# Kernel tuning notes

Measured on AMD Instinct MI355X. Metric: run time of the kernel, lower is better.

## Reference

```python
import jax, jax.numpy as jnp
import numpy as np
import math

B, P, N = 4, 8, 512
D_MODEL, H, D_K = 128, 4, 32
T_ALL = 4
WHICH_IDX = np.array([0, 1, 3])  # which_transition_matrices = [T,T,F,T]
T = 3
EPS = 1e-5


def setup_inputs() -> dict:
    key = jax.random.key(0)
    ks = jax.random.split(key, 12)
    inputs = jax.random.normal(ks[0], (B, P, N, D_MODEL), jnp.float32)
    c_inputs = jax.random.normal(ks[1], (B, P, N, D_MODEL), jnp.float32)
    vals = jax.random.uniform(ks[2], (T_ALL, N, N), jnp.float32)
    keep = (jax.random.uniform(ks[3], (T_ALL, N, N)) < 0.05).astype(jnp.float32)
    eye = jnp.eye(N, dtype=jnp.float32)
    transition_matrices = vals * keep * (1.0 - eye) + eye
    s = 1.0 / math.sqrt(D_MODEL)
    Wq = jax.random.normal(ks[4], (T, D_MODEL, D_MODEL), jnp.float32) * s
    Wk = jax.random.normal(ks[5], (T, D_MODEL, D_MODEL), jnp.float32) * s
    Wv = jax.random.normal(ks[6], (T, D_MODEL, D_MODEL), jnp.float32) * s
    Wo = jax.random.normal(ks[7], (D_MODEL, T * D_MODEL), jnp.float32) * (1.0 / math.sqrt(T * D_MODEL))
    ln_gamma = jnp.ones((D_MODEL,), jnp.float32)
    ln_beta = jnp.zeros((D_MODEL,), jnp.float32)
    return dict(inputs=inputs, c_inputs=c_inputs, transition_matrices=transition_matrices,
                Wq=Wq, Wk=Wk, Wv=Wv, Wo=Wo, ln_gamma=ln_gamma, ln_beta=ln_beta)


def reference(inputs, c_inputs, transition_matrices, Wq, Wk, Wv, Wo, ln_gamma, ln_beta):
    tm = transition_matrices[jnp.asarray(WHICH_IDX)]  # [T, N, N]
    # per-transition-matrix projections (torch Linear: x @ W.T), then split heads
    def proj(W):
        y = jnp.einsum('bpnd,tod->tbpno', inputs, W)
        return y.reshape(T, B, P, N, H, D_K)
    Q, K, V = proj(Wq), proj(Wk), proj(Wv)
    scores = jnp.einsum('tbpnhk,tbpmhk->tbphnm', Q, K) / math.sqrt(D_K)
    mask = jnp.where(tm != 0, 0.0, -jnp.inf)[:, None, None, None]  # [T,1,1,1,N,N]
    alpha = jax.nn.softmax(scores + mask, axis=-1)
    # post-softmax reweighting by transition matrix, then V matmul
    out = jnp.einsum('tbphnm,tbpmhk->tbpnhk', alpha * tm[:, None, None, None], V)
    out = out.reshape(T, B, P, N, D_MODEL)
    out = jnp.moveaxis(out, 0, -2).reshape(B, P, N, T * D_MODEL)  # concat over matrices
    out = jnp.einsum('bpnf,df->bpnd', out, Wo)  # final Linear (bias=False); dropout p=0
    res = out + inputs
    mu = res.mean(-1, keepdims=True)
    var = ((res - mu) ** 2).mean(-1, keepdims=True)
    return (res - mu) / jnp.sqrt(var + EPS) * ln_gamma + ln_beta
```

## Files before the change

kernel.cpp:

```cpp
#include <hip/hip_runtime.h>


typedef __attribute__((ext_vector_type(8))) short  short8;
typedef __attribute__((ext_vector_type(4))) float  floatx4;

#define WS_BIG   50331648ull
#define WS_XL    54919168ull
#define QSCALE   0.25503486f

__device__ __forceinline__ float b2f(unsigned short u) {
    union { unsigned int i; float f; } v; v.i = ((unsigned int)u) << 16; return v.f;
}
__device__ __forceinline__ unsigned short f2b(float f) {
    union { float f; unsigned int i; } v; v.f = f;
    unsigned int x = v.i;
    return (unsigned short)((x + 0x7fffu + ((x >> 16) & 1u)) >> 16);
}
__device__ __forceinline__ unsigned int fbits(float f) {
    union { float f; unsigned int i; } v; v.f = f; return v.i;
}
__device__ __forceinline__ short8 cvt8(const float* p) {
    floatx4 a = *(const floatx4*)p;
    floatx4 b = *(const floatx4*)(p + 4);
    short8 r;
    r[0] = (short)f2b(a[0]); r[1] = (short)f2b(a[1]);
    r[2] = (short)f2b(a[2]); r[3] = (short)f2b(a[3]);
    r[4] = (short)f2b(b[0]); r[5] = (short)f2b(b[1]);
    r[6] = (short)f2b(b[2]); r[7] = (short)f2b(b[3]);
    return r;
}

__global__ __launch_bounds__(256) void k_prep_w(
    const float* __restrict__ Wq, const float* __restrict__ Wk,
    const float* __restrict__ Wv, const float* __restrict__ Wo,
    unsigned short* __restrict__ Wb, unsigned short* __restrict__ Wob)
{
    size_t i = ((size_t)blockIdx.x * 256 + threadIdx.x) * 8;
    const float* src; unsigned short* dst; size_t off;
    if      (i <  49152) { src = Wq; dst = Wb;          off = i; }
    else if (i <  98304) { src = Wk; dst = Wb + 49152;  off = i - 49152; }
    else if (i < 147456) { src = Wv; dst = Wb + 98304;  off = i - 98304; }
    else                 { src = Wo; dst = Wob;         off = i - 147456; }
    *(short8*)&dst[off] = cvt8(&src[off]);
}

__global__ __launch_bounds__(256) void k_qkv_x(
    const float* __restrict__ X,
    const unsigned short* __restrict__ Wb,
    unsigned short* __restrict__ q_ws,
    unsigned short* __restrict__ k_ws,
    unsigned short* __restrict__ v_ws)
{
    int t = blockIdx.x, mt = blockIdx.y, bp = blockIdx.z;
    __shared__ unsigned short Xs[128 * 128];
    __shared__ unsigned short Cs[4][32 * 128];
    int tid = threadIdx.x;
    int lane = tid & 63, wv = tid >> 6;
    int l15 = lane & 15, quad = lane >> 4;

    const float* Xbase = X + ((size_t)bp * 512 + mt * 128) * 128;
    for (int i = 0; i < 8; ++i) {
        int e = (i * 256 + tid) * 8;
        *(short8*)&Xs[e] = cvt8(&Xbase[e]);
    }
    __syncthreads();

    unsigned short* Osel[3] = { q_ws, k_ws, v_ws };
    int rt0 = wv * 2, rt1 = wv * 2 + 1;

    for (int qkv = 0; qkv < 3; ++qkv) {
        const unsigned short* Wt = Wb + qkv * 49152 + t * 16384;
        unsigned short* Ob = Osel[qkv] + (size_t)t * 2097152
                           + ((size_t)bp * 512 + mt * 128 + wv * 32) * 128;
        float sc = (qkv == 0) ? QSCALE : 1.0f;

        for (int ct = 0; ct < 8; ++ct) {
            short8 bfr[4];
            for (int kk = 0; kk < 4; ++kk)
                bfr[kk] = *(const short8*)&Wt[(size_t)(ct * 16 + l15) * 128 + kk * 32 + quad * 8];
            floatx4 acc0 = {0.f, 0.f, 0.f, 0.f};
            floatx4 acc1 = {0.f, 0.f, 0.f, 0.f};
            for (int kk = 0; kk < 4; ++kk) {
                short8 a0 = *(const short8*)&Xs[(rt0 * 16 + l15) * 128 + kk * 32 + quad * 8];
                short8 a1 = *(const short8*)&Xs[(rt1 * 16 + l15) * 128 + kk * 32 + quad * 8];
                acc0 = __builtin_amdgcn_mfma_f32_16x16x32_bf16(a0, bfr[kk], acc0, 0, 0, 0);
                acc1 = __builtin_amdgcn_mfma_f32_16x16x32_bf16(a1, bfr[kk], acc1, 0, 0, 0);
            }
            #pragma unroll
            for (int i = 0; i < 4; ++i) {
                int row = quad * 4 + i;
                int swz = (row & 7) << 4;
                int col = (ct * 16 + l15) ^ swz;
                Cs[wv][row * 128 + col]        = f2b(acc0[i] * sc);
                Cs[wv][(16 + row) * 128 + col] = f2b(acc1[i] * sc);
            }
        }
        #pragma unroll
        for (int j = 0; j < 8; ++j) {
            int flat = j * 64 + lane;
            int r = flat >> 4;
            int cg = (flat & 15) * 8;
            int cgs = cg ^ ((r & 7) << 4);
            *(short8*)&Ob[(size_t)r * 128 + cg] = *(const short8*)&Cs[wv][r * 128 + cgs];
        }
    }
}

__global__ __launch_bounds__(256) void k_qkv_cvt(
    const float* __restrict__ X,
    const float* __restrict__ Wq, const float* __restrict__ Wk,
    const float* __restrict__ Wv,
    unsigned short* __restrict__ q_ws, unsigned short* __restrict__ k_ws,
    unsigned short* __restrict__ v_ws,
    int wstride, int ostride)
{
    int bp = blockIdx.x, mt = blockIdx.y, tz = blockIdx.z;
    __shared__ unsigned short Xs[128 * 128];
    int tid = threadIdx.x;
    int lane = tid & 63, wv = tid >> 6;
    int l15 = lane & 15, quad = lane >> 4;

    const float* Xbase = X + ((size_t)bp * 512 + mt * 128) * 128;
    for (int i = 0; i < 8; ++i) {
        int e = (i * 256 + tid) * 8;
        *(short8*)&Xs[e] = cvt8(&Xbase[e]);
    }
    __syncthreads();

    size_t woff = (size_t)tz * wstride;
    size_t ooff = (size_t)tz * ostride;
    const float* Wsel[3] = { Wq + woff, Wk + woff, Wv + woff };
    unsigned short* Osel[3] = { q_ws + ooff, k_ws + ooff, v_ws + ooff };

    for (int qkv = 0; qkv < 3; ++qkv) {
        const float* Wt = Wsel[qkv];
        unsigned short* Ob = Osel[qkv] + ((size_t)bp * 512 + mt * 128) * 128;
        float sc = (qkv == 0) ? QSCALE : 1.0f;
        for (int ct = 0; ct < 8; ++ct) {
            short8 bfr[4];
            for (int kk = 0; kk < 4; ++kk)
                bfr[kk] = cvt8(&Wt[(size_t)(ct * 16 + l15) * 128 + kk * 32 + quad * 8]);
            floatx4 acc0 = {0.f, 0.f, 0.f, 0.f};
            floatx4 acc1 = {0.f, 0.f, 0.f, 0.f};
            int rt0 = wv * 2, rt1 = wv * 2 + 1;
            for (int kk = 0; kk < 4; ++kk) {
                short8 a0 = *(const short8*)&Xs[(rt0 * 16 + l15) * 128 + kk * 32 + quad * 8];
                short8 a1 = *(const short8*)&Xs[(rt1 * 16 + l15) * 128 + kk * 32 + quad * 8];
                acc0 = __builtin_amdgcn_mfma_f32_16x16x32_bf16(a0, bfr[kk], acc0, 0, 0, 0);
                acc1 = __builtin_amdgcn_mfma_f32_16x16x32_bf16(a1, bfr[kk], acc1, 0, 0, 0);
            }
            int col = ct * 16 + l15;
            for (int i = 0; i < 4; ++i) {
                Ob[(size_t)(rt0 * 16 + quad * 4 + i) * 128 + col] = f2b(acc0[i] * sc);
                Ob[(size_t)(rt1 * 16 + quad * 4 + i) * 128 + col] = f2b(acc1[i] * sc);
            }
        }
    }
}

__global__ __launch_bounds__(512) void k_attn2(
    const unsigned short* __restrict__ q_ws,
    const unsigned short* __restrict__ k_ws,
    const unsigned short* __restrict__ v_ws,
    const float* __restrict__ tm,
    unsigned short* __restrict__ att_ws,
    int qkv_stride, int toff0)
{
    int nc2 = blockIdx.x;
    int bp = blockIdx.y;
    int z  = blockIdx.z;
    int t = z >> 2, h = z & 3;
    size_t qoff = (size_t)t * (size_t)qkv_stride;
    const float* tmt = tm + (size_t)(t + (t >> 1)) * 262144;
    int toff = toff0 + t * 128;

    __shared__ unsigned short Vt[32][516];
    __shared__ unsigned short Ps[8][16][72];

    int tid = threadIdx.x, lane = tid & 63, wv = tid >> 6;
    int l15 = lane & 15, quad = lane >> 4;

    {
        const unsigned short* vp = v_ws + qoff + ((size_t)bp * 512 + tid) * 128 + h * 32;
        short8 a = *(const short8*)vp;
        short8 b = *(const short8*)(vp + 8);
        short8 c = *(const short8*)(vp + 16);
        short8 d = *(const short8*)(vp + 24);
        #pragma unroll
        for (int j = 0; j < 8; ++j) {
            Vt[j][tid]      = (unsigned short)a[j];
            Vt[8 + j][tid]  = (unsigned short)b[j];
            Vt[16 + j][tid] = (unsigned short)c[j];
            Vt[24 + j][tid] = (unsigned short)d[j];
        }
    }
    int n0 = nc2 * 256 + wv * 16;
    short8 qf[2];
    qf[0] = *(const short8*)&q_ws[qoff +
        ((size_t)bp * 512 + n0 + l15) * 128 + h * 32 + quad * 8];
    qf[1] = *(const short8*)&q_ws[qoff +
        ((size_t)bp * 512 + n0 + 128 + l15) * 128 + h * 32 + quad * 8];
    __syncthreads();

    const unsigned short* Kb = k_ws + qoff + (size_t)bp * 512 * 128 + h * 32;
    floatx4 O0[2] = {{0.f,0.f,0.f,0.f},{0.f,0.f,0.f,0.f}};
    floatx4 O1[2] = {{0.f,0.f,0.f,0.f},{0.f,0.f,0.f,0.f}};
    float za[2][4] = {{0.f,0.f,0.f,0.f},{0.f,0.f,0.f,0.f}};
    const floatx4 zero4 = {0.f, 0.f, 0.f, 0.f};

    for (int c = 0; c < 8; ++c) {
        int mb = c * 64;
        short8 kf0 = *(const short8*)&Kb[(size_t)(mb +  0 + l15) * 128 + quad * 8];
        short8 kf1 = *(const short8*)&Kb[(size_t)(mb + 16 + l15) * 128 + quad * 8];
        short8 kf2 = *(const short8*)&Kb[(size_t)(mb + 32 + l15) * 128 + quad * 8];
        short8 kf3 = *(const short8*)&Kb[(size_t)(mb + 48 + l15) * 128 + quad * 8];

        #pragma unroll
        for (int s = 0; s < 2; ++s) {
            int ns = n0 + s * 128;
            floatx4 S[4];
            S[0] = __builtin_amdgcn_mfma_f32_16x16x32_bf16(qf[s], kf0, zero4, 0, 0, 0);
            S[1] = __builtin_amdgcn_mfma_f32_16x16x32_bf16(qf[s], kf1, zero4, 0, 0, 0);
            S[2] = __builtin_amdgcn_mfma_f32_16x16x32_bf16(qf[s], kf2, zero4, 0, 0, 0);
            S[3] = __builtin_amdgcn_mfma_f32_16x16x32_bf16(qf[s], kf3, zero4, 0, 0, 0);

            #pragma unroll
            for (int ti = 0; ti < 4; ++ti) {
                int m = mb + ti * 16 + l15;
                #pragma unroll
                for (int i = 0; i < 4; ++i) {
                    float tmv = tmt[(size_t)(ns + quad * 4 + i) * 512 + m];
                    float e = __builtin_amdgcn_exp2f(S[ti][i]);
                    za[s][i] += (tmv != 0.0f) ? e : 0.0f;
                    float w = e * tmv;
                    Ps[wv][quad * 4 + i][ti * 16 + l15] =
                        (unsigned short)((fbits(w) + 0x8000u) >> 16);
                }
            }
            #pragma unroll
            for (int kc = 0; kc < 2; ++kc) {
                short8 pa  = *(const short8*)&Ps[wv][l15][kc * 32 + quad * 8];
                short8 vb0 = *(const short8*)&Vt[l15][mb + kc * 32 + quad * 8];
                short8 vb1 = *(const short8*)&Vt[16 + l15][mb + kc * 32 + quad * 8];
                O0[s] = __builtin_amdgcn_mfma_f32_16x16x32_bf16(pa, vb0, O0[s], 0, 0, 0);
                O1[s] = __builtin_amdgcn_mfma_f32_16x16x32_bf16(pa, vb1, O1[s], 0, 0, 0);
            }
        }
    }

    #pragma unroll
    for (int s = 0; s < 2; ++s) {
        #pragma unroll
        for (int d = 1; d < 16; d <<= 1) {
            #pragma unroll
            for (int i = 0; i < 4; ++i) za[s][i] += __shfl_xor(za[s][i], d, 64);
        }
        #pragma unroll
        for (int i = 0; i < 4; ++i) {
            float rz = 1.0f / za[s][i];
            size_t row = (size_t)bp * 512 + n0 + s * 128 + quad * 4 + i;
            att_ws[row * 384 + toff + h * 32 + l15]      = f2b(O0[s][i] * rz);
            att_ws[row * 384 + toff + h * 32 + 16 + l15] = f2b(O1[s][i] * rz);
        }
    }
}

__global__ __launch_bounds__(256) void k_oproj_pre(
    const unsigned short* __restrict__ att_ws,
    const unsigned short* __restrict__ Wob,
    const float* __restrict__ X,
    const float* __restrict__ gamma,
    const float* __restrict__ beta,
    float* __restrict__ out)
{
    int bp = blockIdx.x;
    int mt = blockIdx.y;
    __shared__ unsigned short As[64 * 128];
    __shared__ unsigned short Ws[128 * 128];
    int tid = threadIdx.x, lane = tid & 63, wv = tid >> 6;
    int l15 = lane & 15, quad = lane >> 4;

    floatx4 acc[8];
    for (int ct = 0; ct < 8; ++ct) acc[ct] = (floatx4){0.f, 0.f, 0.f, 0.f};
    size_t rowbase = (size_t)bp * 512 + mt * 64;

    for (int kc = 0; kc < 3; ++kc) {
        __syncthreads();
        for (int i = 0; i < 4; ++i) {
            int flat = i * 256 + tid;
            int row = flat >> 4, colg = (flat & 15) * 8;
            *(short8*)&As[row * 128 + colg] =
                *(const short8*)&att_ws[(rowbase + row) * 384 + kc * 128 + colg];
        }
        for (int i = 0; i < 8; ++i) {
            int flat = i * 256 + tid;
            int row = flat >> 4, colg = (flat & 15) * 8;
            *(short8*)&Ws[row * 128 + colg] =
                *(const short8*)&Wob[(size_t)row * 384 + kc * 128 + colg];
        }
        __syncthreads();
        for (int ct = 0; ct < 8; ++ct) {
            for (int kk = 0; kk < 4; ++kk) {
                short8 a = *(const short8*)&As[(wv * 16 + l15) * 128 + kk * 32 + quad * 8];
                short8 b = *(const short8*)&Ws[(ct * 16 + l15) * 128 + kk * 32 + quad * 8];
                acc[ct] = __builtin_amdgcn_mfma_f32_16x16x32_bf16(a, b, acc[ct], 0, 0, 0);
            }
        }
    }

    for (int i = 0; i < 4; ++i) {
        int lrow = wv * 16 + quad * 4 + i;
        size_t grow = rowbase + lrow;
        float vals[8];
        float s = 0.f, sq = 0.f;
        for (int ct = 0; ct < 8; ++ct) {
            int col = ct * 16 + l15;
            float v = acc[ct][i] + X[grow * 128 + col];
            vals[ct] = v;
            s += v; sq += v * v;
        }
        for (int d = 1; d < 16; d <<= 1) {
            s  += __shfl_xor(s, d, 64);
            sq += __shfl_xor(sq, d, 64);
        }
        float mu = s * (1.0f / 128.0f);
        float var = sq * (1.0f / 128.0f) - mu * mu;
        float rs = rsqrtf(var + 1e-5f);
        for (int ct = 0; ct < 8; ++ct) {
            int col = ct * 16 + l15;
            out[grow * 128 + col] = (vals[ct] - mu) * rs * gamma[col] + beta[col];
        }
    }
}

__global__ __launch_bounds__(256) void k_oproj_cvt(
    const unsigned short* __restrict__ att_ws,
    const float* __restrict__ Wo,
    const float* __restrict__ X,
    const float* __restrict__ gamma,
    const float* __restrict__ beta,
    float* __restrict__ out)
{
    int bp = blockIdx.x;
    int mt = blockIdx.y;
    __shared__ unsigned short As[64 * 128];
    __shared__ unsigned short Ws[128 * 128];
    int tid = threadIdx.x, lane = tid & 63, wv = tid >> 6;
    int l15 = lane & 15, quad = lane >> 4;

    floatx4 acc[8];
    for (int ct = 0; ct < 8; ++ct) acc[ct] = (floatx4){0.f, 0.f, 0.f, 0.f};
    size_t rowbase = (size_t)bp * 512 + mt * 64;

    for (int kc = 0; kc < 3; ++kc) {
        __syncthreads();
        for (int i = 0; i < 4; ++i) {
            int flat = i * 256 + tid;
            int row = flat >> 4, colg = (flat & 15) * 8;
            *(short8*)&As[row * 128 + colg] =
                *(const short8*)&att_ws[(rowbase + row) * 384 + kc * 128 + colg];
        }
        for (int i = 0; i < 8; ++i) {
            int flat = i * 256 + tid;
            int row = flat >> 4, colg = (flat & 15) * 8;
            *(short8*)&Ws[row * 128 + colg] = cvt8(&Wo[(size_t)row * 384 + kc * 128 + colg]);
        }
        __syncthreads();
        for (int ct = 0; ct < 8; ++ct) {
            for (int kk = 0; kk < 4; ++kk) {
                short8 a = *(const short8*)&As[(wv * 16 + l15) * 128 + kk * 32 + quad * 8];
                short8 b = *(const short8*)&Ws[(ct * 16 + l15) * 128 + kk * 32 + quad * 8];
                acc[ct] = __builtin_amdgcn_mfma_f32_16x16x32_bf16(a, b, acc[ct], 0, 0, 0);
            }
        }
    }

    for (int i = 0; i < 4; ++i) {
        int lrow = wv * 16 + quad * 4 + i;
        size_t grow = rowbase + lrow;
        float vals[8];
        float s = 0.f, sq = 0.f;
        for (int ct = 0; ct < 8; ++ct) {
            int col = ct * 16 + l15;
            float v = acc[ct][i] + X[grow * 128 + col];
            vals[ct] = v;
            s += v; sq += v * v;
        }
        for (int d = 1; d < 16; d <<= 1) {
            s  += __shfl_xor(s, d, 64);
            sq += __shfl_xor(sq, d, 64);
        }
        float mu = s * (1.0f / 128.0f);
        float var = sq * (1.0f / 128.0f) - mu * mu;
        float rs = rsqrtf(var + 1e-5f);
        for (int ct = 0; ct < 8; ++ct) {
            int col = ct * 16 + l15;
            out[grow * 128 + col] = (vals[ct] - mu) * rs * gamma[col] + beta[col];
        }
    }
}

extern "C" void kernel_launch(void* const* d_in, const int* in_sizes, int n_in,
                              void* d_out, int out_size, void* d_ws, size_t ws_size,
                              hipStream_t stream) {
    const float* X     = (const float*)d_in[0];
    const float* TM    = (const float*)d_in[2];
    const float* Wq    = (const float*)d_in[3];
    const float* Wk    = (const float*)d_in[4];
    const float* Wv    = (const float*)d_in[5];
    const float* Wo    = (const float*)d_in[6];
    const float* gamma = (const float*)d_in[7];
    const float* beta  = (const float*)d_in[8];
    float* out = (float*)d_out;

    char* ws = (char*)d_ws;
    const size_t QKV1 = 2097152;
    const size_t QKV1B = QKV1 * 2;

    if (ws_size >= WS_XL) {
        unsigned short* q3  = (unsigned short*)(ws);
        unsigned short* k3  = (unsigned short*)(ws + 3 * QKV1B);
        unsigned short* v3  = (unsigned short*)(ws + 6 * QKV1B);
        unsigned short* att = (unsigned short*)(ws + 9 * QKV1B);
        unsigned short* Wb  = (unsigned short*)(ws + 50331648ull);
        unsigned short* Wob = (unsigned short*)(ws + 50626560ull);
        k_prep_w<<<dim3(96), 256, 0, stream>>>(Wq, Wk, Wv, Wo, Wb, Wob);
        k_qkv_x<<<dim3(3, 4, 32), 256, 0, stream>>>(X, Wb, q3, k3, v3);
        k_attn2<<<dim3(2, 32, 12), 512, 0, stream>>>(q3, k3, v3, TM, att, (int)QKV1, 0);
        k_oproj_pre<<<dim3(32, 8), 256, 0, stream>>>(att, Wob, X, gamma, beta, out);
    } else if (ws_size >= WS_BIG) {
        unsigned short* q3  = (unsigned short*)(ws);
        unsigned short* k3  = (unsigned short*)(ws + 3 * QKV1B);
        unsigned short* v3  = (unsigned short*)(ws + 6 * QKV1B);
        unsigned short* att = (unsigned short*)(ws + 9 * QKV1B);
        k_qkv_cvt<<<dim3(32, 4, 3), 256, 0, stream>>>(
            X, Wq, Wk, Wv, q3, k3, v3, 16384, (int)QKV1);
        k_attn2<<<dim3(2, 32, 12), 512, 0, stream>>>(q3, k3, v3, TM, att, (int)QKV1, 0);
        k_oproj_cvt<<<dim3(32, 8), 256, 0, stream>>>(att, Wo, X, gamma, beta, out);
    } else {
        unsigned short* q_ws   = (unsigned short*)(ws);
        unsigned short* k_ws   = (unsigned short*)(ws + QKV1B);
        unsigned short* v_ws   = (unsigned short*)(ws + 2 * QKV1B);
        unsigned short* att_ws = (unsigned short*)(ws + 3 * QKV1B);
        const int tsel[3] = {0, 1, 3};
        for (int t = 0; t < 3; ++t) {
            k_qkv_cvt<<<dim3(32, 4, 1), 256, 0, stream>>>(
                X, Wq + (size_t)t * 16384, Wk + (size_t)t * 16384, Wv + (size_t)t * 16384,
                q_ws, k_ws, v_ws, 0, 0);
            k_attn2<<<dim3(2, 32, 4), 512, 0, stream>>>(
                q_ws, k_ws, v_ws, TM + (size_t)tsel[t] * 262144, att_ws, 0, t * 128);
        }
        k_oproj_cvt<<<dim3(32, 8), 256, 0, stream>>>(att_ws, Wo, X, gamma, beta, out);
    }
}
```

Measured before the change: 175.2 us.

## Restructure QKV projection to load X once per block across all transitions

The QKV projection kernel now gives each block a 64-row tile of X and loops over all three transition matrices inside the block, so X is read and converted to bf16 once instead of three times. The A fragments are hoisted into registers and reused across all nine weight matrices. The grid shrinks from 384 to 256 blocks and each wave handles 16 rows instead of 32. That lowers parallelism and leaves less MFMA work per weight-fragment load.

```diff
diff --git a/kernel.cpp b/kernel.cpp
--- a/kernel.cpp
+++ b/kernel.cpp
@@ -44,64 +44,65 @@
     *(short8*)&dst[off] = cvt8(&src[off]);
 }
 
-__global__ __launch_bounds__(256) void k_qkv_x(
+__global__ __launch_bounds__(256) void k_qkv_t(
     const float* __restrict__ X,
     const unsigned short* __restrict__ Wb,
     unsigned short* __restrict__ q_ws,
     unsigned short* __restrict__ k_ws,
     unsigned short* __restrict__ v_ws)
 {
-    int t = blockIdx.x, mt = blockIdx.y, bp = blockIdx.z;
-    __shared__ unsigned short Xs[128 * 128];
-    __shared__ unsigned short Cs[4][32 * 128];
+    int bp = blockIdx.x, nt = blockIdx.y;
+    __shared__ unsigned short Xs[64 * 128];
+    __shared__ unsigned short Cs[4][16 * 128];
     int tid = threadIdx.x;
     int lane = tid & 63, wv = tid >> 6;
     int l15 = lane & 15, quad = lane >> 4;
 
-    const float* Xbase = X + ((size_t)bp * 512 + mt * 128) * 128;
-    for (int i = 0; i < 8; ++i) {
+    const float* Xbase = X + ((size_t)bp * 512 + nt * 64) * 128;
+    for (int i = 0; i < 4; ++i) {
         int e = (i * 256 + tid) * 8;
         *(short8*)&Xs[e] = cvt8(&Xbase[e]);
     }
     __syncthreads();
 
+    short8 af[4];
+    #pragma unroll
+    for (int kk = 0; kk < 4; ++kk)
+        af[kk] = *(const short8*)&Xs[(wv * 16 + l15) * 128 + kk * 32 + quad * 8];
+
     unsigned short* Osel[3] = { q_ws, k_ws, v_ws };
-    int rt0 = wv * 2, rt1 = wv * 2 + 1;
-
-    for (int qkv = 0; qkv < 3; ++qkv) {
-        const unsigned short* Wt = Wb + qkv * 49152 + t * 16384;
-        unsigned short* Ob = Osel[qkv] + (size_t)t * 2097152
-                           + ((size_t)bp * 512 + mt * 128 + wv * 32) * 128;
-        float sc = (qkv == 0) ? QSCALE : 1.0f;
-
-        for (int ct = 0; ct < 8; ++ct) {
-            short8 bfr[4];
-            for (int kk = 0; kk < 4; ++kk)
-                bfr[kk] = *(const short8*)&Wt[(size_t)(ct * 16 + l15) * 128 + kk * 32 + quad * 8];
-            floatx4 acc0 = {0.f, 0.f, 0.f, 0.f};
-            floatx4 acc1 = {0.f, 0.f, 0.f, 0.f};
-            for (int kk = 0; kk < 4; ++kk) {
-                short8 a0 = *(const short8*)&Xs[(rt0 * 16 + l15) * 128 + kk * 32 + quad * 8];
-                short8 a1 = *(const short8*)&Xs[(rt1 * 16 + l15) * 128 + kk * 32 + quad * 8];
-                acc0 = __builtin_amdgcn_mfma_f32_16x16x32_bf16(a0, bfr[kk], acc0, 0, 0, 0);
-                acc1 = __builtin_amdgcn_mfma_f32_16x16x32_bf16(a1, bfr[kk], acc1, 0, 0, 0);
+    size_t obase = ((size_t)bp * 512 + nt * 64 + wv * 16) * 128;
+
+    for (int t = 0; t < 3; ++t) {
+        for (int qkv = 0; qkv < 3; ++qkv) {
+            const unsigned short* Wt = Wb + qkv * 49152 + t * 16384;
+            unsigned short* Ob = Osel[qkv] + (size_t)t * 2097152 + obase;
+            float sc = (qkv == 0) ? QSCALE : 1.0f;
+            for (int ct = 0; ct < 8; ++ct) {
+                short8 bfr[4];
+                #pragma unroll
+                for (int kk = 0; kk < 4; ++kk)
+                    bfr[kk] = *(const short8*)&Wt[(size_t)(ct * 16 + l15) * 128 + kk * 32 + quad * 8];
+                floatx4 acc = {0.f, 0.f, 0.f, 0.f};
+                #pragma unroll
+                for (int kk = 0; kk < 4; ++kk)
+                    acc = __builtin_amdgcn_mfma_f32_16x16x32_bf16(af[kk], bfr[kk], acc, 0, 0, 0);
+                #pragma unroll
+                for (int i = 0; i < 4; ++i) {
+                    int row = quad * 4 + i;
+                    int swz = (row & 7) << 4;
+                    int col = (ct * 16 + l15) ^ swz;
+                    Cs[wv][row * 128 + col] = f2b(acc[i] * sc);
+                }
             }
             #pragma unroll
-            for (int i = 0; i < 4; ++i) {
-                int row = quad * 4 + i;
-                int swz = (row & 7) << 4;
-                int col = (ct * 16 + l15) ^ swz;
-                Cs[wv][row * 128 + col]        = f2b(acc0[i] * sc);
-                Cs[wv][(16 + row) * 128 + col] = f2b(acc1[i] * sc);
-            }
-        }
-        #pragma unroll
-        for (int j = 0; j < 8; ++j) {
-            int flat = j * 64 + lane;
-            int r = flat >> 4;
-            int cg = (flat & 15) * 8;
-            int cgs = cg ^ ((r & 7) << 4);
-            *(short8*)&Ob[(size_t)r * 128 + cg] = *(const short8*)&Cs[wv][r * 128 + cgs];
+            for (int j = 0; j < 4; ++j) {
+                int flat = j * 64 + lane;
+                int r = flat >> 4;
+                int cg = (flat & 15) * 8;
+                int cgs = cg ^ ((r & 7) << 4);
+                *(short8*)&Ob[(size_t)r * 128 + cg] = *(const short8*)&Cs[wv][r * 128 + cgs];
+            }
         }
     }
 }
@@ -425,7 +426,7 @@
         unsigned short* Wb  = (unsigned short*)(ws + 50331648ull);
         unsigned short* Wob = (unsigned short*)(ws + 50626560ull);
         k_prep_w<<<dim3(96), 256, 0, stream>>>(Wq, Wk, Wv, Wo, Wb, Wob);
-        k_qkv_x<<<dim3(3, 4, 32), 256, 0, stream>>>(X, Wb, q3, k3, v3);
+        k_qkv_t<<<dim3(32, 8), 256, 0, stream>>>(X, Wb, q3, k3, v3);
         k_attn2<<<dim3(2, 32, 12), 512, 0, stream>>>(q3, k3, v3, TM, att, (int)QKV1, 0);
         k_oproj_pre<<<dim3(32, 8), 256, 0, stream>>>(att, Wob, X, gamma, beta, out);
     } else if (ws_size >= WS_BIG) {
```

Result: slower. 180.5 us (+3.0%).
